# Kernel tuning notes

Hardware: AMD Instinct MI355X
Metric: run time of the kernel (lower is better)

## Reference

```python
import jax, jax.numpy as jnp
import numpy as np

N_NODES = 100000
N_EDGES = 600000
D_IN = 128
D_OUT = 128
N_REL = 16
N_BASES = 8


def setup_inputs() -> dict:
    key = jax.random.key(0)
    ks = jax.random.split(key, 6)
    x = jax.random.normal(ks[0], (N_NODES, D_IN), dtype=jnp.float32)
    edge_index = jax.random.randint(ks[1], (2, N_EDGES), 0, N_NODES, dtype=jnp.int64)
    edge_type = jax.random.randint(ks[2], (N_EDGES,), 0, N_REL, dtype=jnp.int64)
    # xavier-uniform-ish init scales
    b_lim = float(np.sqrt(6.0 / (D_IN + D_OUT)))
    c_lim = float(np.sqrt(6.0 / (N_REL + N_BASES)))
    w_lim = float(np.sqrt(6.0 / (D_IN + D_OUT)))
    bases = jax.random.uniform(ks[3], (N_BASES, D_IN, D_OUT), jnp.float32, -b_lim, b_lim)
    coefficients = jax.random.uniform(ks[4], (N_REL, N_BASES), jnp.float32, -c_lim, c_lim)
    w_self = jax.random.uniform(ks[5], (D_OUT, D_IN), jnp.float32, -w_lim, w_lim)
    return {"x": x, "edge_index": edge_index, "edge_type": edge_type,
            "bases": bases, "coefficients": coefficients, "w_self": w_self}


def reference(x, edge_index, edge_type, bases, coefficients, w_self):
    # self loop: Linear(in, out, bias=False) -> x @ W^T
    out = x @ w_self.T  # [N, D_OUT]
    # relation weights from basis decomposition
    weights = jnp.einsum('rb,bio->rio', coefficients, bases)  # [R, D_IN, D_OUT]
    row, col = edge_index[0], edge_index[1]
    xc = x[col]  # [E, D_IN] gather of source features
    n_rel = weights.shape[0]
    msg = jnp.zeros((xc.shape[0], w_self.shape[0]), dtype=x.dtype)
    # fixed small loop over relations; masked accumulate matches per-relation grouped GEMM
    for r in range(n_rel):
        sel = (edge_type == r)[:, None]
        msg = msg + jnp.where(sel, xc @ weights[r], jnp.zeros((), x.dtype))
    # scatter-add messages to destination rows
    out = out.at[row].add(msg)
    return out
```

## Files before the change

kernel.cpp:

```cpp
#include <hip/hip_runtime.h>

#define NN 100000
#define NE 600000
#define ET (NE + NN)
#define D 128
#define NREL 16
#define NB 98
#define NBIN (NREL * NB)
#define NBL (NBIN + 1)
#define SCANB 391
#define TPB 4
#define MAXTILES 12544
#define GEMMG ((MAXTILES + TPB - 1) / TPB)
#define WGRID 1088

typedef short short8 __attribute__((ext_vector_type(8)));
typedef float f32x4 __attribute__((ext_vector_type(4)));
typedef unsigned int u32x4 __attribute__((ext_vector_type(4)));

#define C0 0
#define O0 1570
#define CU0 3140
#define T0 4710
#define META_BYTES 25600

#define WT_OFF   0
#define META_OFF 557056
#define DH_OFF   582656
#define TI_OFF   582656
#define DO_OFF   982656
#define DC_OFF   1382664
#define BS_OFF   1782664
#define SSRC_OFF 1784712
#define IDX_OFF  4584712
#define SDST_OFF 7384712
#define XB_OFF   10184712
#define MSG_OFF  35784712
#define NEED_XB  (XB_OFF + (size_t)NN * D * 2)
#define NEED_MSG (MSG_OFF + (size_t)ET * 128 * 2)

__device__ __forceinline__ unsigned short f2bf(float f) {
  unsigned u = __builtin_bit_cast(unsigned, f);
  u += 0x7fffu + ((u >> 16) & 1u);
  return (unsigned short)(u >> 16);
}

__global__ __launch_bounds__(256) void k_ph(const float* __restrict__ bases,
    const float* __restrict__ coef, const float* __restrict__ w_self,
    unsigned short* __restrict__ wT, const float* __restrict__ x,
    unsigned short* __restrict__ xb, const int* __restrict__ ei,
    const int* __restrict__ et, int* __restrict__ meta, int* __restrict__ dstHist,
    int xbf, int doMsg)
{
  int bx = blockIdx.x;
  int tid = threadIdx.x;
  if (bx < WGRID) {
    int idx = bx * 256 + tid;
    int r = idx >> 14;
    int t = idx & 16383;
    float v;
    if (r < 16) {
      int o = t >> 7, i = t & 127;
      float acc = 0.f;
      #pragma unroll
      for (int b = 0; b < 8; ++b)
        acc += coef[r * 8 + b] * bases[b * 16384 + i * 128 + o];
      v = acc;
    } else {
      v = w_self[t];
    }
    wT[idx] = f2bf(v);
    return;
  }
  int hb0 = WGRID + (xbf ? 12500 : 0);
  if (bx < hb0) {
    int i = (bx - WGRID) * 256 + tid;
    if (i >= NN * D / 4) return;
    f32x4 f = __builtin_nontemporal_load((const f32x4*)(x + (size_t)i * 4));
    unsigned short s0 = f2bf(f[0]), s1 = f2bf(f[1]), s2 = f2bf(f[2]), s3 = f2bf(f[3]);
    unsigned long long pk = (unsigned long long)s0 | ((unsigned long long)s1 << 16)
                          | ((unsigned long long)s2 << 32) | ((unsigned long long)s3 << 48);
    *(unsigned long long*)(xb + (size_t)i * 4) = pk;
    return;
  }
  __shared__ int h[NBIN];
  int hb = bx - hb0;
  for (int i = tid; i < NBIN; i += 256) h[i] = 0;
  __syncthreads();
  for (int e = hb * 256 + tid; e < NE; e += 256 * 256) {
    int dst = ei[e];
    atomicAdd(&h[et[e] * NB + (dst >> 10)], 1);
    if (doMsg) atomicAdd(&dstHist[dst], 1);
  }
  __syncthreads();
  for (int i = tid; i < NBIN; i += 256)
    if (h[i]) atomicAdd(&meta[C0 + i], h[i]);
}

__global__ __launch_bounds__(256) void k_scan1(const int* __restrict__ dstHist,
    int* __restrict__ dstOff, int* __restrict__ blockSums)
{
  __shared__ int sh[256];
  int tid = threadIdx.x;
  int d = blockIdx.x * 256 + tid;
  int v = (d < NN) ? (dstHist[d] + 1) : 0;
  sh[tid] = v;
  __syncthreads();
  #pragma unroll
  for (int ofs = 1; ofs < 256; ofs <<= 1) {
    int t = (tid >= ofs) ? sh[tid - ofs] : 0;
    __syncthreads();
    sh[tid] += t;
    __syncthreads();
  }
  if (d < NN) dstOff[d] = sh[tid] - v;
  if (tid == 255) blockSums[blockIdx.x] = sh[tid];
}

__global__ __launch_bounds__(1024) void k_scan2(int* __restrict__ blockSums,
    int* __restrict__ meta, int doMsg)
{
  __shared__ int sA[1024];
  __shared__ int sB[1024];
  int tid = threadIdx.x;

  if (doMsg) {
    int v = (tid < SCANB) ? blockSums[tid] : 0;
    sA[tid] = v;
    __syncthreads();
    #pragma unroll
    for (int ofs = 1; ofs < 1024; ofs <<= 1) {
      int t = (tid >= ofs) ? sA[tid - ofs] : 0;
      __syncthreads();
      sA[tid] += t;
      __syncthreads();
    }
    if (tid < SCANB) blockSums[tid] = sA[tid] - v;
    __syncthreads();
  }

  int i0 = tid * 2, i1 = tid * 2 + 1;
  int c0 = (i0 < NBIN) ? meta[C0 + i0] : ((i0 == NBIN) ? NN : 0);
  int c1 = (i1 < NBIN) ? meta[C0 + i1] : ((i1 == NBIN) ? NN : 0);
  int t0 = (c0 + 63) >> 6, t1 = (c1 + 63) >> 6;
  sA[tid] = c0 + c1;
  sB[tid] = t0 + t1;
  __syncthreads();
  #pragma unroll
  for (int ofs = 1; ofs < 1024; ofs <<= 1) {
    int a = (tid >= ofs) ? sA[tid - ofs] : 0;
    int b = (tid >= ofs) ? sB[tid - ofs] : 0;
    __syncthreads();
    sA[tid] += a;
    sB[tid] += b;
    __syncthreads();
  }
  int offEx = sA[tid] - (c0 + c1);
  int tEx = sB[tid] - (t0 + t1);
  if (i0 < NBL) {
    meta[O0 + i0] = offEx;
    meta[T0 + i0] = tEx;
    if (i0 < NBIN) meta[CU0 + i0] = offEx;
    meta[C0 + i0] = c0;
  }
  if (i1 < NBL) {
    meta[O0 + i1] = offEx + c0;
    meta[T0 + i1] = tEx + t0;
    if (i1 < NBIN) meta[CU0 + i1] = offEx + c0;
    meta[C0 + i1] = c1;
  }
  if (tid == 1023) {
    meta[O0 + NBL] = sA[tid];
    meta[T0 + NBL] = sB[tid];
  }
}

__global__ __launch_bounds__(256) void k_scan3(int* __restrict__ dstOff,
    const int* __restrict__ blockSums, int* __restrict__ dstCursor,
    int* __restrict__ sSrc, int* __restrict__ idx)
{
  int tid = threadIdx.x;
  int d = blockIdx.x * 256 + tid;
  int base = blockSums[blockIdx.x];
  if (d < NN) {
    int o = dstOff[d] + base;
    dstOff[d] = o;
    dstCursor[d] = o + 1;
    idx[o] = NE + d;
    sSrc[NE + d] = d;
  }
  if (d == NN) dstOff[NN] = ET;
}

__global__ __launch_bounds__(256) void k_selfF(int* __restrict__ sSrc, int* __restrict__ sDst)
{
  int n = blockIdx.x * 256 + threadIdx.x;
  if (n < NN) { sSrc[NE + n] = n; sDst[NE + n] = n; }
}

__global__ __launch_bounds__(256) void k_tinfo(const int* __restrict__ meta,
    int4* __restrict__ tinfo)
{
  int t = blockIdx.x * 256 + threadIdx.x;
  if (t >= MAXTILES) return;
  int ntiles = meta[T0 + NBL];
  if (t >= ntiles) { tinfo[t] = make_int4(0, 0, 0, 0); return; }
  int lo = 0, hi = NBL;
  while (lo < hi) {
    int mid = (lo + hi + 1) >> 1;
    if (meta[T0 + mid] <= t) lo = mid; else hi = mid - 1;
  }
  int bin = lo;
  int e0 = meta[O0 + bin] + (t - meta[T0 + bin]) * 64;
  int nr = min(64, meta[O0 + bin + 1] - e0);
  int rel = (bin < NBIN) ? (bin / NB) : 16;
  tinfo[t] = make_int4(e0, nr, rel, 0);
}

__global__ __launch_bounds__(256) void k_scatter(const int* __restrict__ ei, const int* __restrict__ et,
    int* __restrict__ meta, int* __restrict__ sSrc, int* __restrict__ sDst,
    int* __restrict__ dstCursor, int* __restrict__ idx, int doMsg)
{
  __shared__ int h[NBIN], base[NBIN], lh[NBIN];
  int tid = threadIdx.x;
  int start = blockIdx.x * 4096;
  int end = min(NE, start + 4096);
  for (int i = tid; i < NBIN; i += 256) { h[i] = 0; lh[i] = 0; }
  __syncthreads();
  for (int e = start + tid; e < end; e += 256)
    atomicAdd(&h[et[e] * NB + (ei[e] >> 10)], 1);
  __syncthreads();
  for (int i = tid; i < NBIN; i += 256)
    if (h[i]) base[i] = atomicAdd(&meta[CU0 + i], h[i]);
  __syncthreads();
  for (int e = start + tid; e < end; e += 256) {
    int row = ei[e];
    int bin = et[e] * NB + (row >> 10);
    int pos = base[bin] + atomicAdd(&lh[bin], 1);
    sSrc[pos] = ei[NE + e];
    if (doMsg) idx[atomicAdd(&dstCursor[row], 1)] = pos;
    else sDst[pos] = row;
  }
}

__global__ __launch_bounds__(256) void k_gemm(const float* __restrict__ xf,
    const unsigned short* __restrict__ xb,
    const unsigned short* __restrict__ wT, const int* __restrict__ meta,
    const int* __restrict__ sSrc, const int* __restrict__ sDst,
    const int4* __restrict__ tinfo,
    unsigned short* __restrict__ msg, float* __restrict__ out,
    int xbf, int msgmode)
{
  __shared__ short As[64 * 17 * 8];
  __shared__ short Es[64 * 136];
  __shared__ int Rows[64];

  int tid = threadIdx.x;
  int ntiles = meta[T0 + NBL];
  int b0 = blockIdx.x * TPB;
  if (b0 >= ntiles) return;

  int lane = tid & 63, wave = tid >> 6;
  int q = lane >> 4, l15 = lane & 15;
  int m = tid >> 2, ug = tid & 3;

  int rprev = -1;
  short8 bfr[2][4];

  if (xbf && msgmode) {
    for (int ti = 0; ti < TPB; ++ti) {
      int b = b0 + ti;
      if (b >= ntiles) break;
      int4 ifo = tinfo[b];
      int e0 = ifo.x, nr = ifo.y, r = ifo.z;

      bool valid = m < nr;
      int src = sSrc[valid ? (e0 + m) : e0];
      const unsigned short* xr = xb + (size_t)src * 128;
      #pragma unroll
      for (int s = 0; s < 4; ++s) {
        int u = ug * 4 + s;
        short8 pk = (short8)(short)0;
        if (valid) pk = *(const short8*)(xr + u * 8);
        *(short8*)&As[(m * 17 + u) * 8] = pk;
      }
      __syncthreads();

      if (r != rprev) {
        const unsigned short* wr = wT + r * 16384;
        #pragma unroll
        for (int ns = 0; ns < 2; ++ns)
          #pragma unroll
          for (int kk = 0; kk < 4; ++kk)
            bfr[ns][kk] = *(const short8*)(wr + (wave * 32 + ns * 16 + l15) * 128 + kk * 32 + q * 8);
        rprev = r;
      }

      f32x4 acc[4][2];
      #pragma unroll
      for (int ms = 0; ms < 4; ++ms)
        #pragma unroll
        for (int ns = 0; ns < 2; ++ns)
          acc[ms][ns] = (f32x4){0.f, 0.f, 0.f, 0.f};
      #pragma unroll
      for (int kk = 0; kk < 4; ++kk) {
        short8 af[4];
        #pragma unroll
        for (int ms = 0; ms < 4; ++ms)
          af[ms] = *(const short8*)&As[((ms * 16 + l15) * 17 + kk * 4 + q) * 8];
        #pragma unroll
        for (int ms = 0; ms < 4; ++ms)
          #pragma unroll
          for (int ns = 0; ns < 2; ++ns)
            acc[ms][ns] = __builtin_amdgcn_mfma_f32_16x16x32_bf16(af[ms], bfr[ns][kk], acc[ms][ns], 0, 0, 0);
      }

      __syncthreads();
      #pragma unroll
      for (int ms = 0; ms < 4; ++ms)
        #pragma unroll
        for (int ns = 0; ns < 2; ++ns)
          #pragma unroll
          for (int reg = 0; reg < 4; ++reg)
            Es[(ms * 16 + q * 4 + reg) * 136 + wave * 32 + ns * 16 + l15] =
                (short)f2bf(acc[ms][ns][reg]);
      __syncthreads();

      #pragma unroll
      for (int i = 0; i < 4; ++i) {
        int row = wave * 16 + i * 4 + q;
        short8 v = *(const short8*)&Es[row * 136 + l15 * 8];
        if (row < nr)
          *(short8*)(msg + (size_t)(e0 + row) * 128 + l15 * 8) = v;
      }
      __syncthreads();
    }
    return;
  }

  for (int ti = 0; ti < TPB; ++ti) {
    int b = b0 + ti;
    if (b >= ntiles) break;
    int4 ifo = tinfo[b];
    int e0 = ifo.x, nrows = ifo.y, r = ifo.z;

    bool valid = m < nrows;
    int e = valid ? (e0 + m) : e0;
    int src = sSrc[e];
    if (ug == 0) Rows[m] = valid ? sDst[e] : 0;

    if (xbf) {
      const unsigned short* xr = xb + (size_t)src * 128;
      #pragma unroll
      for (int s = 0; s < 4; ++s) {
        int u = ug * 4 + s;
        short8 pk = (short8)(short)0;
        if (valid) pk = *(const short8*)(xr + u * 8);
        *(short8*)&As[(m * 17 + u) * 8] = pk;
      }
    } else {
      const float* xr = xf + (size_t)src * 128;
      #pragma unroll
      for (int s = 0; s < 4; ++s) {
        int u = ug * 4 + s;
        float4 f0 = make_float4(0.f, 0.f, 0.f, 0.f), f1 = f0;
        if (valid) {
          f0 = *(const float4*)(xr + u * 8);
          f1 = *(const float4*)(xr + u * 8 + 4);
        }
        short8 pk;
        pk[0] = (short)f2bf(f0.x); pk[1] = (short)f2bf(f0.y);
        pk[2] = (short)f2bf(f0.z); pk[3] = (short)f2bf(f0.w);
        pk[4] = (short)f2bf(f1.x); pk[5] = (short)f2bf(f1.y);
        pk[6] = (short)f2bf(f1.z); pk[7] = (short)f2bf(f1.w);
        *(short8*)&As[(m * 17 + u) * 8] = pk;
      }
    }
    __syncthreads();

    if (r != rprev) {
      const unsigned short* wr = wT + r * 16384;
      #pragma unroll
      for (int ns = 0; ns < 2; ++ns)
        #pragma unroll
        for (int kk = 0; kk < 4; ++kk)
          bfr[ns][kk] = *(const short8*)(wr + (wave * 32 + ns * 16 + l15) * 128 + kk * 32 + q * 8);
      rprev = r;
    }

    f32x4 acc[4][2];
    #pragma unroll
    for (int ms = 0; ms < 4; ++ms)
      #pragma unroll
      for (int ns = 0; ns < 2; ++ns)
        acc[ms][ns] = (f32x4){0.f, 0.f, 0.f, 0.f};
    #pragma unroll
    for (int kk = 0; kk < 4; ++kk) {
      short8 af[4];
      #pragma unroll
      for (int ms = 0; ms < 4; ++ms)
        af[ms] = *(const short8*)&As[((ms * 16 + l15) * 17 + kk * 4 + q) * 8];
      #pragma unroll
      for (int ms = 0; ms < 4; ++ms)
        #pragma unroll
        for (int ns = 0; ns < 2; ++ns)
          acc[ms][ns] = __builtin_amdgcn_mfma_f32_16x16x32_bf16(af[ms], bfr[ns][kk], acc[ms][ns], 0, 0, 0);
    }

    __syncthreads();
    #pragma unroll
    for (int ms = 0; ms < 4; ++ms)
      #pragma unroll
      for (int reg = 0; reg < 4; ++reg) {
        int mrow = ms * 16 + q * 4 + reg;
        if (mrow < nrows) {
          float* op = out + (size_t)Rows[mrow] * 128 + wave * 32 + l15;
          unsafeAtomicAdd(op, acc[ms][0][reg]);
          unsafeAtomicAdd(op + 16, acc[ms][1][reg]);
        }
      }
    __syncthreads();
  }
}

__global__ __launch_bounds__(256) void k_reduce(const unsigned short* __restrict__ msg,
    const int* __restrict__ dstOff, const int* __restrict__ idx,
    float* __restrict__ out)
{
  int d = blockIdx.x * 16 + (threadIdx.x >> 4);
  if (d >= NN) return;
  int sl = threadIdx.x & 15;
  int s = dstOff[d], e = dstOff[d + 1];
  const unsigned short* base = msg + (size_t)sl * 8;
  float a[8], bacc[8];
  #pragma unroll
  for (int i = 0; i < 8; ++i) { a[i] = 0.f; bacc[i] = 0.f; }
  int j = s;
  for (; j + 1 < e; j += 2) {
    size_t p0 = (size_t)idx[j] * 128;
    size_t p1 = (size_t)idx[j + 1] * 128;
    u32x4 v0 = *(const u32x4*)(base + p0);
    u32x4 v1 = *(const u32x4*)(base + p1);
    #pragma unroll
    for (int c = 0; c < 4; ++c) {
      a[2 * c]     += __builtin_bit_cast(float, v0[c] << 16);
      a[2 * c + 1] += __builtin_bit_cast(float, v0[c] & 0xffff0000u);
      bacc[2 * c]     += __builtin_bit_cast(float, v1[c] << 16);
      bacc[2 * c + 1] += __builtin_bit_cast(float, v1[c] & 0xffff0000u);
    }
  }
  if (j < e) {
    u32x4 v0 = *(const u32x4*)(base + (size_t)idx[j] * 128);
    #pragma unroll
    for (int c = 0; c < 4; ++c) {
      a[2 * c]     += __builtin_bit_cast(float, v0[c] << 16);
      a[2 * c + 1] += __builtin_bit_cast(float, v0[c] & 0xffff0000u);
    }
  }
  f32x4 w0, w1;
  w0[0] = a[0] + bacc[0]; w0[1] = a[1] + bacc[1]; w0[2] = a[2] + bacc[2]; w0[3] = a[3] + bacc[3];
  w1[0] = a[4] + bacc[4]; w1[1] = a[5] + bacc[5]; w1[2] = a[6] + bacc[6]; w1[3] = a[7] + bacc[7];
  float* op = out + (size_t)d * 128 + sl * 8;
  __builtin_nontemporal_store(w0, (f32x4*)op);
  __builtin_nontemporal_store(w1, (f32x4*)(op + 4));
}

extern "C" void kernel_launch(void* const* d_in, const int* in_sizes, int n_in,
                              void* d_out, int out_size, void* d_ws, size_t ws_size,
                              hipStream_t stream)
{
  const float* x      = (const float*)d_in[0];
  const int*   ei     = (const int*)d_in[1];
  const int*   et     = (const int*)d_in[2];
  const float* bases  = (const float*)d_in[3];
  const float* coef   = (const float*)d_in[4];
  const float* w_self = (const float*)d_in[5];
  float* out = (float*)d_out;
  char* ws = (char*)d_ws;
  unsigned short* wT = (unsigned short*)(ws + WT_OFF);
  int* meta      = (int*)(ws + META_OFF);
  int* dstHist   = (int*)(ws + DH_OFF);
  int4* tinfo    = (int4*)(ws + TI_OFF);
  int* dstOff    = (int*)(ws + DO_OFF);
  int* dstCursor = (int*)(ws + DC_OFF);
  int* blockSums = (int*)(ws + BS_OFF);
  int* sSrc      = (int*)(ws + SSRC_OFF);
  int* idx       = (int*)(ws + IDX_OFF);
  int* sDst      = (int*)(ws + SDST_OFF);
  unsigned short* xb = (unsigned short*)(ws + XB_OFF);
  unsigned short* msg = (unsigned short*)(ws + MSG_OFF);

  const int msgmode = (ws_size >= NEED_MSG) ? 1 : 0;
  const int xbf = (msgmode || ws_size >= NEED_XB) ? 1 : 0;

  hipMemsetAsync(ws + META_OFF, 0, META_BYTES + 400000, stream);
  k_ph<<<WGRID + (xbf ? 12500 : 0) + 256, 256, 0, stream>>>(
      bases, coef, w_self, wT, x, xb, ei, et, meta, dstHist, xbf, msgmode);
  if (msgmode) {
    k_scan1<<<SCANB, 256, 0, stream>>>(dstHist, dstOff, blockSums);
    k_scan2<<<1, 1024, 0, stream>>>(blockSums, meta, 1);
    k_scan3<<<SCANB, 256, 0, stream>>>(dstOff, blockSums, dstCursor, sSrc, idx);
  } else {
    k_scan2<<<1, 1024, 0, stream>>>(blockSums, meta, 0);
    k_selfF<<<SCANB, 256, 0, stream>>>(sSrc, sDst);
    hipMemsetAsync(d_out, 0, (size_t)NN * D * 4, stream);
  }
  k_scatter<<<(NE + 4095) / 4096, 256, 0, stream>>>(ei, et, meta, sSrc, sDst, dstCursor, idx, msgmode);
  k_tinfo<<<(MAXTILES + 255) / 256, 256, 0, stream>>>(meta, tinfo);
  k_gemm<<<GEMMG, 256, 0, stream>>>(x, xb, wT, meta, sSrc, sDst, tinfo, msg, out, xbf, msgmode);
  if (msgmode)
    k_reduce<<<(NN + 15) / 16, 256, 0, stream>>>(msg, dstOff, idx, out);
}
```

Before: 345.3 us.

## Bin edges by destination bucket first, interleave self-loops, fuse tinfo into scatter

Edges are now binned by 2048-row destination bucket first and relation second, so each bucket holds its 16 relation groups plus a self-loop group laid out next to each other. This replaces the old relation-major ordering, which used 1024-row buckets and put all self loops at the end. The intent is better locality for the message and scatter writes to destination rows, and fewer bins to scan. The tile-info binary search is folded into extra blocks of the scatter kernel, which removes one kernel launch. The trade-off is that tiles are now smaller per bin, so more partially filled tiles and relation switches may occur in the GEMM.

```diff
diff --git a/kernel.cpp b/kernel.cpp
--- a/kernel.cpp
+++ b/kernel.cpp
@@ -5,13 +5,17 @@
 #define ET (NE + NN)
 #define D 128
 #define NREL 16
-#define NB 98
-#define NBIN (NREL * NB)
-#define NBL (NBIN + 1)
+#define BSH 11
+#define BSZ 2048
+#define NB 49
+#define BPB 17
+#define NBIN (NB * BPB)
 #define SCANB 391
 #define TPB 4
 #define MAXTILES 12544
 #define GEMMG ((MAXTILES + TPB - 1) / TPB)
+#define SCATB ((NE + 4095) / 4096)
+#define TIB ((MAXTILES + 255) / 256)
 #define WGRID 1088
 
 typedef short short8 __attribute__((ext_vector_type(8)));
@@ -19,23 +23,23 @@
 typedef unsigned int u32x4 __attribute__((ext_vector_type(4)));
 
 #define C0 0
-#define O0 1570
-#define CU0 3140
-#define T0 4710
-#define META_BYTES 25600
+#define O0 840
+#define CU0 1680
+#define T0 2520
+#define META_BYTES 13568
 
 #define WT_OFF   0
 #define META_OFF 557056
-#define DH_OFF   582656
-#define TI_OFF   582656
-#define DO_OFF   982656
-#define DC_OFF   1382664
-#define BS_OFF   1782664
-#define SSRC_OFF 1784712
-#define IDX_OFF  4584712
-#define SDST_OFF 7384712
-#define XB_OFF   10184712
-#define MSG_OFF  35784712
+#define DH_OFF   570624
+#define TI_OFF   570624
+#define DO_OFF   970624
+#define DC_OFF   1370640
+#define BS_OFF   1770640
+#define SSRC_OFF 1772688
+#define IDX_OFF  4572688
+#define SDST_OFF 7372688
+#define XB_OFF   10172688
+#define MSG_OFF  35772688
 #define NEED_XB  (XB_OFF + (size_t)NN * D * 2)
 #define NEED_MSG (MSG_OFF + (size_t)ET * 128 * 2)
 
@@ -89,7 +93,7 @@
   __syncthreads();
   for (int e = hb * 256 + tid; e < NE; e += 256 * 256) {
     int dst = ei[e];
-    atomicAdd(&h[et[e] * NB + (dst >> 10)], 1);
+    atomicAdd(&h[(dst >> BSH) * BPB + et[e]], 1);
     if (doMsg) atomicAdd(&dstHist[dst], 1);
   }
   __syncthreads();
@@ -139,12 +143,15 @@
     __syncthreads();
   }
 
-  int i0 = tid * 2, i1 = tid * 2 + 1;
-  int c0 = (i0 < NBIN) ? meta[C0 + i0] : ((i0 == NBIN) ? NN : 0);
-  int c1 = (i1 < NBIN) ? meta[C0 + i1] : ((i1 == NBIN) ? NN : 0);
-  int t0 = (c0 + 63) >> 6, t1 = (c1 + 63) >> 6;
-  sA[tid] = c0 + c1;
-  sB[tid] = t0 + t1;
+  int c = 0;
+  if (tid < NBIN) {
+    int rel = tid % BPB;
+    if (rel == 16) c = min(BSZ, NN - (tid / BPB) * BSZ);
+    else c = meta[C0 + tid];
+  }
+  int t = (c + 63) >> 6;
+  sA[tid] = c;
+  sB[tid] = t;
   __syncthreads();
   #pragma unroll
   for (int ofs = 1; ofs < 1024; ofs <<= 1) {
@@ -155,29 +162,18 @@
     sB[tid] += b;
     __syncthreads();
   }
-  int offEx = sA[tid] - (c0 + c1);
-  int tEx = sB[tid] - (t0 + t1);
-  if (i0 < NBL) {
-    meta[O0 + i0] = offEx;
-    meta[T0 + i0] = tEx;
-    if (i0 < NBIN) meta[CU0 + i0] = offEx;
-    meta[C0 + i0] = c0;
-  }
-  if (i1 < NBL) {
-    meta[O0 + i1] = offEx + c0;
-    meta[T0 + i1] = tEx + t0;
-    if (i1 < NBIN) meta[CU0 + i1] = offEx + c0;
-    meta[C0 + i1] = c1;
-  }
-  if (tid == 1023) {
-    meta[O0 + NBL] = sA[tid];
-    meta[T0 + NBL] = sB[tid];
+  int offEx = sA[tid] - c;
+  int tEx = sB[tid] - t;
+  if (tid <= NBIN) {
+    meta[O0 + tid] = offEx;
+    meta[T0 + tid] = tEx;
+    if (tid < NBIN) meta[CU0 + tid] = offEx;
   }
 }
 
 __global__ __launch_bounds__(256) void k_scan3(int* __restrict__ dstOff,
     const int* __restrict__ blockSums, int* __restrict__ dstCursor,
-    int* __restrict__ sSrc, int* __restrict__ idx)
+    int* __restrict__ sSrc, int* __restrict__ idx, const int* __restrict__ meta)
 {
   int tid = threadIdx.x;
   int d = blockIdx.x * 256 + tid;
@@ -186,56 +182,65 @@
     int o = dstOff[d] + base;
     dstOff[d] = o;
     dstCursor[d] = o + 1;
-    idx[o] = NE + d;
-    sSrc[NE + d] = d;
+    int bkt = d >> BSH;
+    int selfPos = meta[O0 + bkt * BPB + 16] + (d & (BSZ - 1));
+    idx[o] = selfPos;
+    sSrc[selfPos] = d;
   }
   if (d == NN) dstOff[NN] = ET;
 }
 
-__global__ __launch_bounds__(256) void k_selfF(int* __restrict__ sSrc, int* __restrict__ sDst)
+__global__ __launch_bounds__(256) void k_selfF(int* __restrict__ sSrc, int* __restrict__ sDst,
+    const int* __restrict__ meta)
 {
   int n = blockIdx.x * 256 + threadIdx.x;
-  if (n < NN) { sSrc[NE + n] = n; sDst[NE + n] = n; }
-}
-
-__global__ __launch_bounds__(256) void k_tinfo(const int* __restrict__ meta,
-    int4* __restrict__ tinfo)
-{
-  int t = blockIdx.x * 256 + threadIdx.x;
-  if (t >= MAXTILES) return;
-  int ntiles = meta[T0 + NBL];
-  if (t >= ntiles) { tinfo[t] = make_int4(0, 0, 0, 0); return; }
-  int lo = 0, hi = NBL;
-  while (lo < hi) {
-    int mid = (lo + hi + 1) >> 1;
-    if (meta[T0 + mid] <= t) lo = mid; else hi = mid - 1;
-  }
-  int bin = lo;
-  int e0 = meta[O0 + bin] + (t - meta[T0 + bin]) * 64;
-  int nr = min(64, meta[O0 + bin + 1] - e0);
-  int rel = (bin < NBIN) ? (bin / NB) : 16;
-  tinfo[t] = make_int4(e0, nr, rel, 0);
+  if (n < NN) {
+    int bkt = n >> BSH;
+    int selfPos = meta[O0 + bkt * BPB + 16] + (n & (BSZ - 1));
+    sSrc[selfPos] = n;
+    sDst[selfPos] = n;
+  }
 }
 
 __global__ __launch_bounds__(256) void k_scatter(const int* __restrict__ ei, const int* __restrict__ et,
     int* __restrict__ meta, int* __restrict__ sSrc, int* __restrict__ sDst,
-    int* __restrict__ dstCursor, int* __restrict__ idx, int doMsg)
+    int* __restrict__ dstCursor, int* __restrict__ idx, int4* __restrict__ tinfo,
+    int doMsg)
 {
   __shared__ int h[NBIN], base[NBIN], lh[NBIN];
   int tid = threadIdx.x;
-  int start = blockIdx.x * 4096;
+  int bx = blockIdx.x;
+
+  if (bx >= SCATB) {
+    int t = (bx - SCATB) * 256 + tid;
+    if (t >= MAXTILES) return;
+    int ntiles = meta[T0 + NBIN];
+    if (t >= ntiles) { tinfo[t] = make_int4(0, 0, 0, 0); return; }
+    int lo = 0, hi = NBIN;
+    while (lo < hi) {
+      int mid = (lo + hi + 1) >> 1;
+      if (meta[T0 + mid] <= t) lo = mid; else hi = mid - 1;
+    }
+    int bin = lo;
+    int e0 = meta[O0 + bin] + (t - meta[T0 + bin]) * 64;
+    int nr = min(64, meta[O0 + bin + 1] - e0);
+    tinfo[t] = make_int4(e0, nr, bin % BPB, 0);
+    return;
+  }
+
+  int start = bx * 4096;
   int end = min(NE, start + 4096);
   for (int i = tid; i < NBIN; i += 256) { h[i] = 0; lh[i] = 0; }
   __syncthreads();
   for (int e = start + tid; e < end; e += 256)
-    atomicAdd(&h[et[e] * NB + (ei[e] >> 10)], 1);
+    atomicAdd(&h[(ei[e] >> BSH) * BPB + et[e]], 1);
   __syncthreads();
   for (int i = tid; i < NBIN; i += 256)
     if (h[i]) base[i] = atomicAdd(&meta[CU0 + i], h[i]);
   __syncthreads();
   for (int e = start + tid; e < end; e += 256) {
     int row = ei[e];
-    int bin = et[e] * NB + (row >> 10);
+    int bin = (row >> BSH) * BPB + et[e];
     int pos = base[bin] + atomicAdd(&lh[bin], 1);
     sSrc[pos] = ei[NE + e];
     if (doMsg) idx[atomicAdd(&dstCursor[row], 1)] = pos;
@@ -256,7 +261,7 @@
   __shared__ int Rows[64];
 
   int tid = threadIdx.x;
-  int ntiles = meta[T0 + NBL];
+  int ntiles = meta[T0 + NBIN];
   int b0 = blockIdx.x * TPB;
   if (b0 >= ntiles) return;
 
@@ -499,14 +504,13 @@
   if (msgmode) {
     k_scan1<<<SCANB, 256, 0, stream>>>(dstHist, dstOff, blockSums);
     k_scan2<<<1, 1024, 0, stream>>>(blockSums, meta, 1);
-    k_scan3<<<SCANB, 256, 0, stream>>>(dstOff, blockSums, dstCursor, sSrc, idx);
+    k_scan3<<<SCANB, 256, 0, stream>>>(dstOff, blockSums, dstCursor, sSrc, idx, meta);
   } else {
     k_scan2<<<1, 1024, 0, stream>>>(blockSums, meta, 0);
-    k_selfF<<<SCANB, 256, 0, stream>>>(sSrc, sDst);
+    k_selfF<<<SCANB, 256, 0, stream>>>(sSrc, sDst, meta);
     hipMemsetAsync(d_out, 0, (size_t)NN * D * 4, stream);
   }
-  k_scatter<<<(NE + 4095) / 4096, 256, 0, stream>>>(ei, et, meta, sSrc, sDst, dstCursor, idx, msgmode);
-  k_tinfo<<<(MAXTILES + 255) / 256, 256, 0, stream>>>(meta, tinfo);
+  k_scatter<<<SCATB + TIB, 256, 0, stream>>>(ei, et, meta, sSrc, sDst, dstCursor, idx, tinfo, msgmode);
   k_gemm<<<GEMMG, 256, 0, stream>>>(x, xb, wT, meta, sSrc, sDst, tinfo, msg, out, xbf, msgmode);
   if (msgmode)
     k_reduce<<<(NN + 15) / 16, 256, 0, stream>>>(msg, dstOff, idx, out);
```

Measured after the change: 336.8 us. 1.03x faster.
